# Performance work log

Measured on AMD Instinct MI355X. Metric: run time of the kernel, lower is better.

## Reference

```python
import jax, jax.numpy as jnp
import numpy as np

N_NODES = 50000
N_EDGES = 800000
N_FEAT = 128
N_HID = 256
N_PAIRS = 100000


def _gcn_norm(edge_index, n_nodes):
    # add self loops, compute D^-1/2 (A+I) D^-1/2 edge weights (PyG gcn_norm)
    loops = jnp.arange(n_nodes, dtype=edge_index.dtype)
    row = jnp.concatenate([edge_index[0], loops])
    col = jnp.concatenate([edge_index[1], loops])
    deg = jax.ops.segment_sum(jnp.ones_like(col, dtype=jnp.float32), col,
                              num_segments=n_nodes)
    dinv = jnp.where(deg > 0, jax.lax.rsqrt(deg), 0.0)
    norm = dinv[row] * dinv[col]  # [E + N]
    return row, col, norm


def _gcn_conv(x, W, b, row, col, norm, n_nodes):
    h = x @ W                       # [N, out]
    msg = h[row] * norm[:, None]    # gather + scale  [E+N, out]
    agg = jax.ops.segment_sum(msg, col, num_segments=n_nodes)  # scatter-add
    return agg + b


def setup_inputs() -> dict:
    key = jax.random.key(0)
    ks = jax.random.split(key, 9)
    edge_index = jax.random.randint(ks[0], (2, N_EDGES), 0, N_NODES, dtype=jnp.int64)
    features = jax.random.normal(ks[1], (N_NODES, N_FEAT), dtype=jnp.float32)
    mask = jax.random.randint(ks[2], (N_PAIRS, 2), 0, N_NODES, dtype=jnp.int64)
    s1 = 1.0 / np.sqrt(N_FEAT)
    s2 = 1.0 / np.sqrt(N_HID)
    W1 = jax.random.uniform(ks[3], (N_FEAT, N_HID), jnp.float32, -s1, s1)
    b1 = jnp.zeros((N_HID,), jnp.float32)
    W2 = jax.random.uniform(ks[4], (N_HID, N_FEAT), jnp.float32, -s2, s2)
    b2 = jnp.zeros((N_FEAT,), jnp.float32)
    Wl = jax.random.uniform(ks[5], (N_HID, 1), jnp.float32, -s2, s2)
    bl = jax.random.uniform(ks[6], (1,), jnp.float32, -s2, s2)
    return {"edge_index": edge_index, "features": features, "mask": mask,
            "W1": W1, "b1": b1, "W2": W2, "b2": b2, "Wl": Wl, "bl": bl}


def reference(edge_index, features, mask, W1, b1, W2, b2, Wl, bl):
    n = features.shape[0]
    row, col, norm = _gcn_norm(edge_index, n)
    h = _gcn_conv(features, W1, b1, row, col, norm, n)   # GCNConv a
    h = jax.nn.relu(h)                                   # dropout p=0 -> identity
    h = _gcn_conv(h, W2, b2, row, col, norm, n)          # GCNConv b
    mt = mask.T
    p1 = jax.lax.stop_gradient(h[mt[0]])                 # .detach()
    p2 = jax.lax.stop_gradient(h[mt[1]])
    hp = jnp.concatenate([p1, p2], axis=1)               # [n_pairs, 2*n_feat]
    return jax.nn.sigmoid(hp @ Wl + bl)
```

## Files before the change

### kernel.cpp

```cpp
#include <hip/hip_runtime.h>
#include <math.h>

#define NFEAT 128
#define NHID 256
#define NBLK 128

typedef __attribute__((ext_vector_type(8))) short short8;
typedef __attribute__((ext_vector_type(4))) float f32x4;

__device__ inline unsigned short f2bf(float f) {
  unsigned u = __float_as_uint(f);
  u += 0x7fffu + ((u >> 16) & 1u);
  return (unsigned short)(u >> 16);
}
__device__ inline float bflo(unsigned u) { return __uint_as_float(u << 16); }
__device__ inline float bfhi(unsigned u) { return __uint_as_float(u & 0xffff0000u); }


__device__ inline void packOne(const float* __restrict__ W,
                               unsigned short* __restrict__ Wp, int idx, int KS,
                               int OUT) {
  int lane = idx & 63;
  int t = idx >> 6;
  int ks = t % KS;
  int nt = t / KS;
  int n = nt * 16 + (lane & 15);
  int k0 = ks * 32 + (lane >> 4) * 8;
  unsigned short v[8];
#pragma unroll
  for (int j = 0; j < 8; j++) v[j] = f2bf(W[(size_t)(k0 + j) * OUT + n]);
  *reinterpret_cast<short8*>(Wp + (size_t)idx * 8) =
      *reinterpret_cast<short8*>(v);
}

__global__ __launch_bounds__(1024) void k_hist_pack(
    const int* __restrict__ col, int* __restrict__ hist2d, int nE, int nb,
    const float* __restrict__ W1, const float* __restrict__ W2,
    unsigned short* __restrict__ W1p, unsigned short* __restrict__ W2p) {
  if (blockIdx.x >= NBLK) {
    int idx = (blockIdx.x - NBLK) * 1024 + threadIdx.x;
    if (idx < 4096) packOne(W1, W1p, idx, 4, 256);
    else packOne(W2, W2p, idx - 4096, 8, 128);
    return;
  }
  __shared__ int h[1024];
  for (int i = threadIdx.x; i < nb; i += 1024) h[i] = 0;
  __syncthreads();
  int chunk = (nE + NBLK - 1) / NBLK;
  int beg = blockIdx.x * chunk, end = min(beg + chunk, nE);
  for (int e = beg + threadIdx.x; e < end; e += 1024)
    atomicAdd(&h[col[e] >> 6], 1);
  __syncthreads();
  for (int i = threadIdx.x; i < nb; i += 1024)
    hist2d[i * NBLK + blockIdx.x] = h[i];
}

__global__ __launch_bounds__(256) void k_bsum(const int* __restrict__ a,
                                              int* __restrict__ psum, int S) {
  int i = blockIdx.x * 256 + threadIdx.x;
  int v = (i < S) ? a[i] : 0;
#pragma unroll
  for (int o = 32; o; o >>= 1) v += __shfl_down(v, o);
  __shared__ int ws[4];
  if ((threadIdx.x & 63) == 0) ws[threadIdx.x >> 6] = v;
  __syncthreads();
  if (threadIdx.x == 0) psum[blockIdx.x] = ws[0] + ws[1] + ws[2] + ws[3];
}

__global__ __launch_bounds__(256) void k_s3m(const int* __restrict__ a,
                                             const int* __restrict__ psum,
                                             int* __restrict__ out, int S) {
  __shared__ int sh[256];
  __shared__ int ws[4];
  int t = threadIdx.x;
  int b = blockIdx.x;
  int partial = 0;
  for (int i = t; i < b; i += 256) partial += psum[i];
#pragma unroll
  for (int o = 32; o; o >>= 1) partial += __shfl_down(partial, o);
  if ((t & 63) == 0) ws[t >> 6] = partial;
  int i = b * 256 + t;
  int d = (i < S) ? a[i] : 0;
  sh[t] = d;
  __syncthreads();
  int base = ws[0] + ws[1] + ws[2] + ws[3];
  for (int o = 1; o < 256; o <<= 1) {
    int u = (t >= o) ? sh[t - o] : 0;
    __syncthreads();
    sh[t] += u;
    __syncthreads();
  }
  if (i < S) out[i] = base + sh[t] - d;
}

__global__ __launch_bounds__(1024) void k_part2(const int* __restrict__ row,
                                                const int* __restrict__ col,
                                                const int* __restrict__ sbase,
                                                unsigned* __restrict__ tmp,
                                                int nE, int nb) {
  __shared__ int cur[1024];
  for (int i = threadIdx.x; i < nb; i += 1024)
    cur[i] = sbase[i * NBLK + blockIdx.x];
  __syncthreads();
  int chunk = (nE + NBLK - 1) / NBLK;
  int beg = blockIdx.x * chunk, end = min(beg + chunk, nE);
  for (int e = beg + threadIdx.x; e < end; e += 1024) {
    int c = col[e];
    int pos = atomicAdd(&cur[c >> 6], 1);
    tmp[pos] = ((unsigned)(c & 63) << 16) | (unsigned)row[e];
  }
}

__global__ __launch_bounds__(256) void k_bsort_cvt(
    const unsigned* __restrict__ tmp, const int* __restrict__ sbase,
    int* __restrict__ ebuf, int* __restrict__ offs, float* __restrict__ dinv,
    const float* __restrict__ feat, unsigned short* __restrict__ xs, int n,
    int nE, int nb) {
  __shared__ int bins[64], cur[64];
  __shared__ float sdinv[64];
  int b = blockIdx.x;
  int beg = sbase[b * NBLK];
  int end = (b == nb - 1) ? nE : sbase[(b + 1) * NBLK];
  int t = threadIdx.x;
  if (t == 0 && b == nb - 1) offs[n] = nE;
  if (t < 64) bins[t] = 0;
  __syncthreads();
  for (int i = beg + t; i < end; i += 256) atomicAdd(&bins[tmp[i] >> 16], 1);
  __syncthreads();
  if (t < 64) {
    int v = bins[t];
    int s = v;
#pragma unroll
    for (int o = 1; o < 64; o <<= 1) {
      int u = __shfl_up(s, o);
      if (t >= o) s += u;
    }
    int off = beg + s - v;
    cur[t] = off;
    float dv = rsqrtf((float)(v + 1));
    sdinv[t] = dv;
    int node = b * 64 + t;
    if (node < n) {
      offs[node] = off;
      dinv[node] = dv;
    }
  }
  __syncthreads();
  for (int i = beg + t; i < end; i += 256) {
    unsigned p = tmp[i];
    int pos = atomicAdd(&cur[p >> 16], 1);
    ebuf[pos] = (int)(p & 0xffffu);
  }
  for (int i = t; i < 64 * 32; i += 256) {
    int r = i >> 5;
    int node = b * 64 + r;
    if (node >= n) break;
    float d = sdinv[r];
    float4 v = reinterpret_cast<const float4*>(feat)[(size_t)node * 32 + (i & 31)];
    unsigned short o[4] = {f2bf(v.x * d), f2bf(v.y * d), f2bf(v.z * d),
                           f2bf(v.w * d)};
    reinterpret_cast<ushort4*>(xs)[(size_t)node * 32 + (i & 31)] =
        *reinterpret_cast<ushort4*>(o);
  }
}

__global__ __launch_bounds__(256) void k_agg_bf(
    const unsigned int* __restrict__ G, const int* __restrict__ offs,
    const int* __restrict__ ebuf, const float* __restrict__ dinv,
    unsigned int* __restrict__ OUTP, int n) {
  int node = blockIdx.x * 4 + (threadIdx.x >> 6);
  if (node >= n) return;
  int lane = threadIdx.x & 63;
  int g = lane >> 4;
  int c = lane & 15;
  int beg = offs[node], end = offs[node + 1];
  float acc[8];
  if (g == 0) {
    uint4 s = *reinterpret_cast<const uint4*>(G + (size_t)node * 64 + c * 4);
    acc[0] = bflo(s.x); acc[1] = bfhi(s.x); acc[2] = bflo(s.y); acc[3] = bfhi(s.y);
    acc[4] = bflo(s.z); acc[5] = bfhi(s.z); acc[6] = bflo(s.w); acc[7] = bfhi(s.w);
  } else {
#pragma unroll
    for (int j = 0; j < 8; j++) acc[j] = 0.f;
  }
  for (int e = beg + g; e < end; e += 4) {
    int src = ebuf[e];
    uint4 v = *reinterpret_cast<const uint4*>(G + (size_t)src * 64 + c * 4);
    acc[0] += bflo(v.x); acc[1] += bfhi(v.x);
    acc[2] += bflo(v.y); acc[3] += bfhi(v.y);
    acc[4] += bflo(v.z); acc[5] += bfhi(v.z);
    acc[6] += bflo(v.w); acc[7] += bfhi(v.w);
  }
#pragma unroll
  for (int j = 0; j < 8; j++) {
    acc[j] += __shfl_down(acc[j], 32);
    acc[j] += __shfl_down(acc[j], 16);
  }
  if (g == 0) {
    float d = dinv[node];
    unsigned o[4];
#pragma unroll
    for (int k = 0; k < 4; k++)
      o[k] = (unsigned)f2bf(acc[2 * k] * d) |
             ((unsigned)f2bf(acc[2 * k + 1] * d) << 16);
    *reinterpret_cast<uint4*>(OUTP + (size_t)node * 64 + c * 4) =
        *reinterpret_cast<uint4*>(o);
  }
}

__global__ __launch_bounds__(256) void k_agg_q(
    const unsigned int* __restrict__ G, const int* __restrict__ offs,
    const int* __restrict__ ebuf, const float* __restrict__ dinv,
    const float* __restrict__ b2, const float* __restrict__ Wl,
    float2* __restrict__ q, int n) {
  int node = blockIdx.x * 4 + (threadIdx.x >> 6);
  if (node >= n) return;
  int lane = threadIdx.x & 63;
  int g = lane >> 4;
  int c = lane & 15;
  int beg = offs[node], end = offs[node + 1];
  float acc[8];
  if (g == 0) {
    uint4 s = *reinterpret_cast<const uint4*>(G + (size_t)node * 64 + c * 4);
    acc[0] = bflo(s.x); acc[1] = bfhi(s.x); acc[2] = bflo(s.y); acc[3] = bfhi(s.y);
    acc[4] = bflo(s.z); acc[5] = bfhi(s.z); acc[6] = bflo(s.w); acc[7] = bfhi(s.w);
  } else {
#pragma unroll
    for (int j = 0; j < 8; j++) acc[j] = 0.f;
  }
  for (int e = beg + g; e < end; e += 4) {
    int src = ebuf[e];
    uint4 v = *reinterpret_cast<const uint4*>(G + (size_t)src * 64 + c * 4);
    acc[0] += bflo(v.x); acc[1] += bfhi(v.x);
    acc[2] += bflo(v.y); acc[3] += bfhi(v.y);
    acc[4] += bflo(v.z); acc[5] += bfhi(v.z);
    acc[6] += bflo(v.w); acc[7] += bfhi(v.w);
  }
#pragma unroll
  for (int j = 0; j < 8; j++) {
    acc[j] += __shfl_down(acc[j], 32);
    acc[j] += __shfl_down(acc[j], 16);
  }
  if (g == 0) {
    float d = dinv[node];
    float q1 = 0.f, q2 = 0.f;
#pragma unroll
    for (int j = 0; j < 8; j++) {
      float hf = acc[j] * d + b2[c * 8 + j];
      q1 += hf * Wl[c * 8 + j];
      q2 += hf * Wl[128 + c * 8 + j];
    }
#pragma unroll
    for (int o = 8; o; o >>= 1) {
      q1 += __shfl_xor(q1, o);
      q2 += __shfl_xor(q2, o);
    }
    if (c == 0) q[node] = make_float2(q1, q2);
  }
}

__global__ __launch_bounds__(256) void k_mfma_fused(
    const unsigned short* __restrict__ A, const unsigned short* __restrict__ B1p,
    const unsigned short* __restrict__ B2p, const float* __restrict__ b1,
    const float* __restrict__ dinv, unsigned short* __restrict__ G2) {
  __shared__ unsigned short sh1[32 * 264];
  int rt0 = blockIdx.x * 2;
  int wave = threadIdx.x >> 6;
  int lane = threadIdx.x & 63;
  int quad = lane >> 4;
  int mrow0 = rt0 * 16 + (lane & 15);

  f32x4 acc[2][4] = {};
  const short8* Ap0 =
      reinterpret_cast<const short8*>(A + (size_t)mrow0 * NFEAT + quad * 8);
  const short8* Ap1 = reinterpret_cast<const short8*>(
      A + (size_t)(mrow0 + 16) * NFEAT + quad * 8);
#pragma unroll
  for (int ks = 0; ks < 4; ks++) {
    short8 a0 = Ap0[ks * 4];
    short8 a1 = Ap1[ks * 4];
#pragma unroll
    for (int ct = 0; ct < 4; ct++) {
      int nt = wave * 4 + ct;
      short8 b = *reinterpret_cast<const short8*>(
          B1p + ((size_t)(nt * 4 + ks) * 64 + lane) * 8);
      acc[0][ct] = __builtin_amdgcn_mfma_f32_16x16x32_bf16(a0, b, acc[0][ct], 0, 0, 0);
      acc[1][ct] = __builtin_amdgcn_mfma_f32_16x16x32_bf16(a1, b, acc[1][ct], 0, 0, 0);
    }
  }
#pragma unroll
  for (int ct = 0; ct < 4; ct++) {
    int c = (wave * 4 + ct) * 16 + (lane & 15);
    float bv = b1[c];
#pragma unroll
    for (int rg = 0; rg < 2; rg++)
#pragma unroll
      for (int i = 0; i < 4; i++) {
        float v = fmaxf(acc[rg][ct][i] + bv, 0.f);
        sh1[(rg * 16 + quad * 4 + i) * 264 + c] = f2bf(v);
      }
  }
  __syncthreads();

  f32x4 acc2[2][2] = {};
  const unsigned short* a2_0 = sh1 + (size_t)(lane & 15) * 264 + quad * 8;
  const unsigned short* a2_1 = sh1 + (size_t)(16 + (lane & 15)) * 264 + quad * 8;
#pragma unroll
  for (int ks = 0; ks < 8; ks++) {
    short8 a0 = *reinterpret_cast<const short8*>(a2_0 + ks * 32);
    short8 a1 = *reinterpret_cast<const short8*>(a2_1 + ks * 32);
#pragma unroll
    for (int ct = 0; ct < 2; ct++) {
      int nt = wave * 2 + ct;
      short8 b = *reinterpret_cast<const short8*>(
          B2p + ((size_t)(nt * 8 + ks) * 64 + lane) * 8);
      acc2[0][ct] = __builtin_amdgcn_mfma_f32_16x16x32_bf16(a0, b, acc2[0][ct], 0, 0, 0);
      acc2[1][ct] = __builtin_amdgcn_mfma_f32_16x16x32_bf16(a1, b, acc2[1][ct], 0, 0, 0);
    }
  }
#pragma unroll
  for (int rg = 0; rg < 2; rg++) {
    int r0 = (rt0 + rg) * 16 + quad * 4;
    float dv[4];
#pragma unroll
    for (int i = 0; i < 4; i++) dv[i] = dinv[r0 + i];
#pragma unroll
    for (int ct = 0; ct < 2; ct++) {
      int c = (wave * 2 + ct) * 16 + (lane & 15);
#pragma unroll
      for (int i = 0; i < 4; i++)
        G2[(size_t)(r0 + i) * NFEAT + c] = f2bf(acc2[rg][ct][i] * dv[i]);
    }
  }
}

__global__ __launch_bounds__(256) void k_head2(const float2* __restrict__ q,
                                               const int* __restrict__ mask,
                                               const float* __restrict__ bl,
                                               float* __restrict__ out, int P) {
  int p = blockIdx.x * 256 + threadIdx.x;
  if (p >= P) return;
  int m0 = mask[2 * p], m1 = mask[2 * p + 1];
  float s = q[m0].x + q[m1].y + bl[0];
  out[p] = 1.0f / (1.0f + expf(-s));
}

extern "C" void kernel_launch(void* const* d_in, const int* in_sizes, int n_in,
                              void* d_out, int out_size, void* d_ws,
                              size_t ws_size, hipStream_t stream) {
  const int* edge = (const int*)d_in[0];
  const float* feat = (const float*)d_in[1];
  const int* mask = (const int*)d_in[2];
  const float* W1 = (const float*)d_in[3];
  const float* b1 = (const float*)d_in[4];
  const float* W2 = (const float*)d_in[5];
  const float* b2 = (const float*)d_in[6];
  const float* Wl = (const float*)d_in[7];
  const float* bl = (const float*)d_in[8];
  float* out = (float*)d_out;

  const int E = in_sizes[0] / 2;
  const int N = in_sizes[1] / NFEAT;
  const int P = in_sizes[2] / 2;
  const int* rowp = edge;
  const int* colp = edge + E;
  const int nrt = N / 16;
  const int nb = (N + 63) / 64;
  const int S = nb * NBLK;
  const int nS = (S + 255) / 256;

  auto aln = [](size_t x) { return (x + 255) & ~(size_t)255; };
  const size_t rowSlack = (size_t)16 * NFEAT * 2;
  char* w = (char*)d_ws;
  int* hist2d = (int*)w;           w += aln((size_t)S * 4);
  int* sbase = (int*)w;            w += aln((size_t)S * 4);
  int* psum = (int*)w;             w += aln((size_t)1024 * 4);
  int* offs = (int*)w;             w += aln((size_t)(N + 1) * 4);
  int* ebuf = (int*)w;             w += aln((size_t)E * 4);
  unsigned* tmp = (unsigned*)w;    w += aln((size_t)E * 4);
  float* dinv = (float*)w;         w += aln((size_t)N * 4 + 1024);
  unsigned short* xs = (unsigned short*)w;  w += aln((size_t)N * NFEAT * 2);
  unsigned short* z = (unsigned short*)w;   w += aln((size_t)N * NFEAT * 2 + rowSlack);
  unsigned short* g2 = (unsigned short*)w;  w += aln((size_t)N * NFEAT * 2 + rowSlack);
  float2* q = (float2*)w;          w += aln((size_t)N * 8);
  unsigned short* W1p = (unsigned short*)w; w += aln((size_t)NFEAT * NHID * 2);
  unsigned short* W2p = (unsigned short*)w; w += aln((size_t)NHID * NFEAT * 2);

  k_hist_pack<<<NBLK + 8, 1024, 0, stream>>>(colp, hist2d, E, nb, W1, W2, W1p,
                                             W2p);
  k_bsum<<<nS, 256, 0, stream>>>(hist2d, psum, S);
  k_s3m<<<nS, 256, 0, stream>>>(hist2d, psum, sbase, S);
  k_part2<<<NBLK, 1024, 0, stream>>>(rowp, colp, sbase, tmp, E, nb);
  k_bsort_cvt<<<nb, 256, 0, stream>>>(tmp, sbase, ebuf, offs, dinv, feat, xs,
                                      N, E, nb);
  k_agg_bf<<<(N + 3) / 4, 256, 0, stream>>>((const unsigned*)xs, offs, ebuf,
                                            dinv, (unsigned*)z, N);
  k_mfma_fused<<<(nrt + 1) / 2, 256, 0, stream>>>(z, W1p, W2p, b1, dinv, g2);
  k_agg_q<<<(N + 3) / 4, 256, 0, stream>>>((const unsigned*)g2, offs, ebuf,
                                           dinv, b2, Wl, q, N);
  k_head2<<<(P + 255) / 256, 256, 0, stream>>>(q, mask, bl, out, P);
}
```

Before: 206.8 us.

## Project layer-2 output onto head weights before aggregation to aggregate scalars

Because the second GCN aggregation and the linear head are both linear, the head weights are applied per node inside the fused MFMA kernel, producing two scalars per node instead of a 128-wide bf16 row. The second aggregation then sums float2 values per node instead of gathering 256-byte rows, and the bias term b2·Wl+bl is folded into a constant computed in a spare block of k_bsum. This removes the 128-wide feature write and the wide gather traffic of the old k_agg_q. In exchange it adds shared-memory atomics and shuffle reductions in the MFMA epilogue, and it changes the rounding order because the projected values are no longer rounded to bf16.

New measurement: 178.2 us. -13.8%, faster.

```diff
diff --git a/kernel.cpp b/kernel.cpp
--- a/kernel.cpp
+++ b/kernel.cpp
@@ -56,15 +56,30 @@
 }
 
 __global__ __launch_bounds__(256) void k_bsum(const int* __restrict__ a,
-                                              int* __restrict__ psum, int S) {
-  int i = blockIdx.x * 256 + threadIdx.x;
+                                              int* __restrict__ psum, int S,
+                                              const float* __restrict__ b2,
+                                              const float* __restrict__ Wl,
+                                              const float* __restrict__ bl,
+                                              float* __restrict__ Cbuf) {
+  int t = threadIdx.x;
+  if (blockIdx.x == gridDim.x - 1) {
+    float v = (t < 128) ? b2[t] * (Wl[t] + Wl[128 + t]) : 0.f;
+#pragma unroll
+    for (int o = 32; o; o >>= 1) v += __shfl_down(v, o);
+    __shared__ float fw[4];
+    if ((t & 63) == 0) fw[t >> 6] = v;
+    __syncthreads();
+    if (t == 0) Cbuf[0] = fw[0] + fw[1] + fw[2] + fw[3] + bl[0];
+    return;
+  }
+  int i = blockIdx.x * 256 + t;
   int v = (i < S) ? a[i] : 0;
 #pragma unroll
   for (int o = 32; o; o >>= 1) v += __shfl_down(v, o);
   __shared__ int ws[4];
-  if ((threadIdx.x & 63) == 0) ws[threadIdx.x >> 6] = v;
-  __syncthreads();
-  if (threadIdx.x == 0) psum[blockIdx.x] = ws[0] + ws[1] + ws[2] + ws[3];
+  if ((t & 63) == 0) ws[t >> 6] = v;
+  __syncthreads();
+  if (t == 0) psum[blockIdx.x] = ws[0] + ws[1] + ws[2] + ws[3];
 }
 
 __global__ __launch_bounds__(256) void k_s3m(const int* __restrict__ a,
@@ -208,67 +223,19 @@
   }
 }
 
-__global__ __launch_bounds__(256) void k_agg_q(
-    const unsigned int* __restrict__ G, const int* __restrict__ offs,
-    const int* __restrict__ ebuf, const float* __restrict__ dinv,
-    const float* __restrict__ b2, const float* __restrict__ Wl,
-    float2* __restrict__ q, int n) {
-  int node = blockIdx.x * 4 + (threadIdx.x >> 6);
-  if (node >= n) return;
-  int lane = threadIdx.x & 63;
-  int g = lane >> 4;
-  int c = lane & 15;
-  int beg = offs[node], end = offs[node + 1];
-  float acc[8];
-  if (g == 0) {
-    uint4 s = *reinterpret_cast<const uint4*>(G + (size_t)node * 64 + c * 4);
-    acc[0] = bflo(s.x); acc[1] = bfhi(s.x); acc[2] = bflo(s.y); acc[3] = bfhi(s.y);
-    acc[4] = bflo(s.z); acc[5] = bfhi(s.z); acc[6] = bflo(s.w); acc[7] = bfhi(s.w);
-  } else {
-#pragma unroll
-    for (int j = 0; j < 8; j++) acc[j] = 0.f;
-  }
-  for (int e = beg + g; e < end; e += 4) {
-    int src = ebuf[e];
-    uint4 v = *reinterpret_cast<const uint4*>(G + (size_t)src * 64 + c * 4);
-    acc[0] += bflo(v.x); acc[1] += bfhi(v.x);
-    acc[2] += bflo(v.y); acc[3] += bfhi(v.y);
-    acc[4] += bflo(v.z); acc[5] += bfhi(v.z);
-    acc[6] += bflo(v.w); acc[7] += bfhi(v.w);
-  }
-#pragma unroll
-  for (int j = 0; j < 8; j++) {
-    acc[j] += __shfl_down(acc[j], 32);
-    acc[j] += __shfl_down(acc[j], 16);
-  }
-  if (g == 0) {
-    float d = dinv[node];
-    float q1 = 0.f, q2 = 0.f;
-#pragma unroll
-    for (int j = 0; j < 8; j++) {
-      float hf = acc[j] * d + b2[c * 8 + j];
-      q1 += hf * Wl[c * 8 + j];
-      q2 += hf * Wl[128 + c * 8 + j];
-    }
-#pragma unroll
-    for (int o = 8; o; o >>= 1) {
-      q1 += __shfl_xor(q1, o);
-      q2 += __shfl_xor(q2, o);
-    }
-    if (c == 0) q[node] = make_float2(q1, q2);
-  }
-}
-
 __global__ __launch_bounds__(256) void k_mfma_fused(
     const unsigned short* __restrict__ A, const unsigned short* __restrict__ B1p,
     const unsigned short* __restrict__ B2p, const float* __restrict__ b1,
-    const float* __restrict__ dinv, unsigned short* __restrict__ G2) {
+    const float* __restrict__ dinv, const float* __restrict__ Wl,
+    float* __restrict__ P) {
   __shared__ unsigned short sh1[32 * 264];
+  __shared__ float pacc[32][2];
   int rt0 = blockIdx.x * 2;
   int wave = threadIdx.x >> 6;
   int lane = threadIdx.x & 63;
   int quad = lane >> 4;
   int mrow0 = rt0 * 16 + (lane & 15);
+  if (threadIdx.x < 64) pacc[threadIdx.x >> 1][threadIdx.x & 1] = 0.f;
 
   f32x4 acc[2][4] = {};
   const short8* Ap0 =
@@ -318,6 +285,7 @@
       acc2[1][ct] = __builtin_amdgcn_mfma_f32_16x16x32_bf16(a1, b, acc2[1][ct], 0, 0, 0);
     }
   }
+  float p1[2][4] = {}, p2[2][4] = {};
 #pragma unroll
   for (int rg = 0; rg < 2; rg++) {
     int r0 = (rt0 + rg) * 16 + quad * 4;
@@ -327,21 +295,75 @@
 #pragma unroll
     for (int ct = 0; ct < 2; ct++) {
       int c = (wave * 2 + ct) * 16 + (lane & 15);
-#pragma unroll
-      for (int i = 0; i < 4; i++)
-        G2[(size_t)(r0 + i) * NFEAT + c] = f2bf(acc2[rg][ct][i] * dv[i]);
-    }
-  }
+      float wl1 = Wl[c], wl2 = Wl[128 + c];
+#pragma unroll
+      for (int i = 0; i < 4; i++) {
+        float v = acc2[rg][ct][i] * dv[i];
+        p1[rg][i] = fmaf(v, wl1, p1[rg][i]);
+        p2[rg][i] = fmaf(v, wl2, p2[rg][i]);
+      }
+    }
+  }
+#pragma unroll
+  for (int rg = 0; rg < 2; rg++)
+#pragma unroll
+    for (int i = 0; i < 4; i++) {
+#pragma unroll
+      for (int o = 8; o; o >>= 1) {
+        p1[rg][i] += __shfl_xor(p1[rg][i], o);
+        p2[rg][i] += __shfl_xor(p2[rg][i], o);
+      }
+    }
+  if ((lane & 15) == 0) {
+#pragma unroll
+    for (int rg = 0; rg < 2; rg++)
+#pragma unroll
+      for (int i = 0; i < 4; i++) {
+        int row = rg * 16 + quad * 4 + i;
+        atomicAdd(&pacc[row][0], p1[rg][i]);
+        atomicAdd(&pacc[row][1], p2[rg][i]);
+      }
+  }
+  __syncthreads();
+  if (threadIdx.x < 64) {
+    int row = threadIdx.x >> 1, comp = threadIdx.x & 1;
+    P[(size_t)(rt0 * 16 + row) * 2 + comp] = pacc[row][comp];
+  }
+}
+
+__global__ __launch_bounds__(256) void k_agg_s(const float2* __restrict__ p,
+                                               const int* __restrict__ offs,
+                                               const int* __restrict__ ebuf,
+                                               const float* __restrict__ dinv,
+                                               float2* __restrict__ q, int n) {
+  int i = blockIdx.x * 256 + threadIdx.x;
+  if (i >= n) return;
+  int beg = offs[i], end = offs[i + 1];
+  float2 s = p[i];
+  int e = beg;
+  for (; e + 4 <= end; e += 4) {
+    int s0 = ebuf[e], s1 = ebuf[e + 1], s2 = ebuf[e + 2], s3 = ebuf[e + 3];
+    float2 v0 = p[s0], v1 = p[s1], v2 = p[s2], v3 = p[s3];
+    s.x += v0.x + v1.x + v2.x + v3.x;
+    s.y += v0.y + v1.y + v2.y + v3.y;
+  }
+  for (; e < end; e++) {
+    float2 v = p[ebuf[e]];
+    s.x += v.x;
+    s.y += v.y;
+  }
+  float d = dinv[i];
+  q[i] = make_float2(s.x * d, s.y * d);
 }
 
 __global__ __launch_bounds__(256) void k_head2(const float2* __restrict__ q,
                                                const int* __restrict__ mask,
-                                               const float* __restrict__ bl,
+                                               const float* __restrict__ Cbuf,
                                                float* __restrict__ out, int P) {
   int p = blockIdx.x * 256 + threadIdx.x;
   if (p >= P) return;
   int m0 = mask[2 * p], m1 = mask[2 * p + 1];
-  float s = q[m0].x + q[m1].y + bl[0];
+  float s = q[m0].x + q[m1].y + Cbuf[0];
   out[p] = 1.0f / (1.0f + expf(-s));
 }
 
@@ -375,28 +397,29 @@
   int* hist2d = (int*)w;           w += aln((size_t)S * 4);
   int* sbase = (int*)w;            w += aln((size_t)S * 4);
   int* psum = (int*)w;             w += aln((size_t)1024 * 4);
+  float* Cbuf = (float*)w;         w += aln(256);
   int* offs = (int*)w;             w += aln((size_t)(N + 1) * 4);
   int* ebuf = (int*)w;             w += aln((size_t)E * 4);
   unsigned* tmp = (unsigned*)w;    w += aln((size_t)E * 4);
   float* dinv = (float*)w;         w += aln((size_t)N * 4 + 1024);
   unsigned short* xs = (unsigned short*)w;  w += aln((size_t)N * NFEAT * 2);
   unsigned short* z = (unsigned short*)w;   w += aln((size_t)N * NFEAT * 2 + rowSlack);
-  unsigned short* g2 = (unsigned short*)w;  w += aln((size_t)N * NFEAT * 2 + rowSlack);
+  float* p = (float*)w;            w += aln((size_t)(N + 32) * 8);
   float2* q = (float2*)w;          w += aln((size_t)N * 8);
   unsigned short* W1p = (unsigned short*)w; w += aln((size_t)NFEAT * NHID * 2);
   unsigned short* W2p = (unsigned short*)w; w += aln((size_t)NHID * NFEAT * 2);
 
   k_hist_pack<<<NBLK + 8, 1024, 0, stream>>>(colp, hist2d, E, nb, W1, W2, W1p,
                                              W2p);
-  k_bsum<<<nS, 256, 0, stream>>>(hist2d, psum, S);
+  k_bsum<<<nS + 1, 256, 0, stream>>>(hist2d, psum, S, b2, Wl, bl, Cbuf);
   k_s3m<<<nS, 256, 0, stream>>>(hist2d, psum, sbase, S);
   k_part2<<<NBLK, 1024, 0, stream>>>(rowp, colp, sbase, tmp, E, nb);
   k_bsort_cvt<<<nb, 256, 0, stream>>>(tmp, sbase, ebuf, offs, dinv, feat, xs,
                                       N, E, nb);
   k_agg_bf<<<(N + 3) / 4, 256, 0, stream>>>((const unsigned*)xs, offs, ebuf,
                                             dinv, (unsigned*)z, N);
-  k_mfma_fused<<<(nrt + 1) / 2, 256, 0, stream>>>(z, W1p, W2p, b1, dinv, g2);
-  k_agg_q<<<(N + 3) / 4, 256, 0, stream>>>((const unsigned*)g2, offs, ebuf,
-                                           dinv, b2, Wl, q, N);
-  k_head2<<<(P + 255) / 256, 256, 0, stream>>>(q, mask, bl, out, P);
-}
+  k_mfma_fused<<<(nrt + 1) / 2, 256, 0, stream>>>(z, W1p, W2p, b1, dinv, Wl, p);
+  k_agg_s<<<(N + 255) / 256, 256, 0, stream>>>((const float2*)p, offs, ebuf,
+                                               dinv, q, N);
+  k_head2<<<(P + 255) / 256, 256, 0, stream>>>(q, mask, Cbuf, out, P);
+}
```
